# Kernel tuning notes

Measured on AMD Instinct MI355X. Metric: run time of the kernel, lower is better.

Reference implementation:

```python
import jax, jax.numpy as jnp
import numpy as np

VOCAB = 32000
WDIM = 768      # bert-base hidden size, per self.w_dim
H = 512         # lstm_hidden
NUM_CAT = 5
START = 3       # l2ind['SOS']
END = 4         # l2ind['EOS']
T = 2048
NEG = -10000.0


def _lstm_dir(x, Wih, Whh, bih, bhh, reverse):
    # x: [T, WDIM]; torch LSTM gate order: i, f, g, o
    z_in = x @ Wih.T + bih + bhh  # [T, 4H] precompute input projection
    def step(carry, zt):
        h, c = carry
        z = zt + h @ Whh.T
        i, f, g, o = jnp.split(z, 4)
        c = jax.nn.sigmoid(f) * c + jax.nn.sigmoid(i) * jnp.tanh(g)
        h = jax.nn.sigmoid(o) * jnp.tanh(c)
        return (h, c), h
    init = (jnp.zeros((H,), x.dtype), jnp.zeros((H,), x.dtype))
    _, hs = jax.lax.scan(step, init, z_in, reverse=reverse)
    return hs  # [T, H], aligned with input order


def setup_inputs():
    key = jax.random.key(0)
    ks = jax.random.split(key, 13)
    s = 0.05
    sent = jax.random.randint(ks[0], (T,), 0, VOCAB)
    emb = jax.random.normal(ks[1], (VOCAB, WDIM), jnp.float32) * 0.02
    Wih_f = jax.random.normal(ks[2], (4 * H, WDIM), jnp.float32) * s
    Whh_f = jax.random.normal(ks[3], (4 * H, H), jnp.float32) * s
    bih_f = jax.random.normal(ks[4], (4 * H,), jnp.float32) * s
    bhh_f = jax.random.normal(ks[5], (4 * H,), jnp.float32) * s
    Wih_b = jax.random.normal(ks[6], (4 * H, WDIM), jnp.float32) * s
    Whh_b = jax.random.normal(ks[7], (4 * H, H), jnp.float32) * s
    bih_b = jax.random.normal(ks[8], (4 * H,), jnp.float32) * s
    bhh_b = jax.random.normal(ks[9], (4 * H,), jnp.float32) * s
    fc_w = jax.random.normal(ks[10], (NUM_CAT, 2 * H), jnp.float32) * s
    fc_b = jax.random.normal(ks[11], (NUM_CAT,), jnp.float32) * s
    transitions = jax.random.normal(ks[12], (NUM_CAT, NUM_CAT), jnp.float32)
    transitions = transitions.at[START, :].set(NEG).at[:, END].set(NEG)
    return {"sent": sent, "emb": emb,
            "Wih_f": Wih_f, "Whh_f": Whh_f, "bih_f": bih_f, "bhh_f": bhh_f,
            "Wih_b": Wih_b, "Whh_b": Whh_b, "bih_b": bih_b, "bhh_b": bhh_b,
            "fc_w": fc_w, "fc_b": fc_b, "transitions": transitions}


def reference(sent, emb, Wih_f, Whh_f, bih_f, bhh_f, Wih_b, Whh_b, bih_b, bhh_b, fc_w, fc_b, transitions):
    # _get_scores: embedding -> BiLSTM -> fc
    x = emb[sent]                                   # [T, WDIM]
    h_f = _lstm_dir(x, Wih_f, Whh_f, bih_f, bhh_f, reverse=False)
    h_b = _lstm_dir(x, Wih_b, Whh_b, bih_b, bhh_b, reverse=True)
    out = jnp.concatenate([h_f, h_b], axis=-1)      # [T, 2H]
    feats = out @ fc_w.T + fc_b                     # [T, NUM_CAT]

    # _viterbi_decode: transitions[i, j] = score of moving from tag j to tag i
    init = feats[0] + transitions[:, START]         # [NUM_CAT]
    def vstep(layer, feat_t):
        # scores[i, j] = feat_t[i] + transitions[i, j] + layer[j]
        scores = feat_t[:, None] + transitions + layer[None, :]
        return jnp.max(scores, axis=1), jnp.argmax(scores, axis=1)
    layer, parents = jax.lax.scan(vstep, init, feats[1:])  # parents: [T-1, NUM_CAT]

    final = layer + transitions[END]
    idx0 = jnp.argmax(final)
    path_score = jnp.max(final)

    # backtrack (parents[0] of the original loop is all-START and gets popped)
    def btrack(idx, p):
        nxt = p[idx]
        return nxt, nxt
    _, idxs = jax.lax.scan(btrack, idx0, parents, reverse=True)  # [T-1]
    path = jnp.concatenate([idxs, idx0[None]])      # [T]
    return path, path_score
```

## Files before the change

### kernel.cpp

```cpp
#include <hip/hip_runtime.h>

#define TT 2048
#define WD 768
#define HH 512
#define G4 2048
#define NC 5
#define SENT 0xFFFFFFFFu

typedef float f4 __attribute__((ext_vector_type(4)));
typedef unsigned int u4 __attribute__((ext_vector_type(4)));

__global__ __launch_bounds__(256, 1) void fused_main(
    const int* __restrict__ sent, const float* __restrict__ emb,
    const float* __restrict__ Wih_f, const float* __restrict__ bih_f, const float* __restrict__ bhh_f,
    const float* __restrict__ Wih_b, const float* __restrict__ bih_b, const float* __restrict__ bhh_b,
    const float* __restrict__ Whh_f, const float* __restrict__ Whh_b,
    float* __restrict__ zin_f, float* __restrict__ zin_b,
    unsigned int* __restrict__ hw_f, unsigned int* __restrict__ hw_b,
    unsigned int* __restrict__ zcnt)
{
    __shared__ float As[16][128];
    __shared__ float Bs[16][128];
    __shared__ float hs[HH];
    __shared__ float zb[256];

    const int tid = threadIdx.x;

    if (blockIdx.x >= 64) {
        const int lin  = blockIdx.x - 64;
        const int pair = lin >> 5;
        const int sub  = lin & 31;
        const int dirn = sub & 1;
        const int gx   = sub >> 1;
        const int ty   = dirn ? (15 - pair) : pair;

        const float* Wih = dirn ? Wih_b : Wih_f;
        const float* bih = dirn ? bih_b : bih_f;
        const float* bhh = dirn ? bhh_b : bhh_f;
        float* zin = dirn ? zin_b : zin_f;

        const int t0 = ty * 128;
        const int g0 = gx * 128;
        const int tm = tid >> 4, tn = tid & 15;

        float acc[8][8];
#pragma unroll
        for (int a = 0; a < 8; a++)
#pragma unroll
            for (int b = 0; b < 8; b++) acc[a][b] = 0.f;

        for (int kt = 0; kt < 48; ++kt) {
            const int k0 = kt * 16;
#pragma unroll
            for (int u = 0; u < 2; ++u) {
                const int s = tid * 2 + u;
                const int m = s >> 2, kq = s & 3;
                const int rowA = sent[t0 + m];
                float4 av = *(const float4*)(emb + (size_t)rowA * WD + k0 + kq * 4);
                As[kq * 4 + 0][m] = av.x; As[kq * 4 + 1][m] = av.y;
                As[kq * 4 + 2][m] = av.z; As[kq * 4 + 3][m] = av.w;
                float4 bv = *(const float4*)(Wih + (size_t)(g0 + m) * WD + k0 + kq * 4);
                Bs[kq * 4 + 0][m] = bv.x; Bs[kq * 4 + 1][m] = bv.y;
                Bs[kq * 4 + 2][m] = bv.z; Bs[kq * 4 + 3][m] = bv.w;
            }
            __syncthreads();
#pragma unroll
            for (int kk = 0; kk < 16; ++kk) {
                float4 a0 = *(const float4*)&As[kk][tm * 8];
                float4 a1 = *(const float4*)&As[kk][tm * 8 + 4];
                float4 b0 = *(const float4*)&Bs[kk][tn * 8];
                float4 b1 = *(const float4*)&Bs[kk][tn * 8 + 4];
                float av8[8] = {a0.x, a0.y, a0.z, a0.w, a1.x, a1.y, a1.z, a1.w};
                float bv8[8] = {b0.x, b0.y, b0.z, b0.w, b1.x, b1.y, b1.z, b1.w};
#pragma unroll
                for (int a = 0; a < 8; a++)
#pragma unroll
                    for (int b = 0; b < 8; b++) acc[a][b] += av8[a] * bv8[b];
            }
            __syncthreads();
        }
        float bias[8];
#pragma unroll
        for (int b = 0; b < 8; b++) { int g = g0 + tn * 8 + b; bias[b] = bih[g] + bhh[g]; }
#pragma unroll
        for (int a = 0; a < 8; a++) {
            const int t = t0 + tm * 8 + a;
            float* op = zin + (size_t)t * G4 + g0 + tn * 8;
            f4 o0 = {acc[a][0] + bias[0], acc[a][1] + bias[1], acc[a][2] + bias[2], acc[a][3] + bias[3]};
            f4 o1 = {acc[a][4] + bias[4], acc[a][5] + bias[5], acc[a][6] + bias[6], acc[a][7] + bias[7]};
            asm volatile("global_store_dwordx4 %0, %1, off sc1" :: "v"(op), "v"(o0) : "memory");
            asm volatile("global_store_dwordx4 %0, %1, off sc1" :: "v"(op + 4), "v"(o1) : "memory");
        }
        __syncthreads();
        if (tid == 0) atomicAdd(&zcnt[dirn * 16 + ty], 1u);
        return;
    }

    const int bid = blockIdx.x;
    const int d = bid >> 5;
    const int k = bid & 31;
    const float* zin = d ? zin_b : zin_f;
    const float* Whh = d ? Whh_b : Whh_f;
    unsigned int* hw = d ? hw_b : hw_f;

    const int q = tid >> 6;
    const int r = tid & 63;
    const int gate = r >> 4, jj = r & 15;
    const int grow = gate * HH + k * 16 + jj;

    const f4* wp = (const f4*)(Whh + (size_t)grow * HH + q * 128);
    f4 w[32];
#pragma unroll
    for (int i = 0; i < 32; ++i) w[i] = wp[i];
#pragma unroll
    for (int i = 0; i < 32; ++i)
        asm volatile("" : "+a"(w[i]));

    float c = 0.f;
    const int l = tid;
    const int g = l >> 4, j = l & 15;
    const int n16 = k * 16 + j;

    int readyty = -1;

    for (int it = 0; it < TT; ++it) {
        const int t = d ? (TT - 1 - it) : it;

        float z = 0.f;
        if (tid < 64) {
            const int tyc = t >> 7;
            if (tyc != readyty) {
                const unsigned int* cp = zcnt + d * 16 + tyc;
                unsigned int cv;
                do {
                    asm volatile("global_load_dword %0, %1, off sc0 sc1\n\t"
                                 "s_waitcnt vmcnt(0)"
                                 : "=v"(cv) : "v"(cp) : "memory");
                } while (cv < 16u);
                readyty = tyc;
            }
            z = zin[(size_t)t * G4 + g * HH + n16];
        }

        if (it > 0 && tid < 64) {
            const int tp = d ? (t + 1) : (t - 1);
            const unsigned int* pa = hw + (size_t)tp * HH + l * 8;
            u4 a0, a1;
            for (;;) {
                asm volatile(
                    "global_load_dwordx4 %0, %2, off sc0 sc1\n\t"
                    "global_load_dwordx4 %1, %2, off offset:16 sc0 sc1\n\t"
                    "s_waitcnt vmcnt(0)"
                    : "=v"(a0), "=v"(a1) : "v"(pa) : "memory");
                if (a0.x != SENT && a0.y != SENT && a0.z != SENT && a0.w != SENT &&
                    a1.x != SENT && a1.y != SENT && a1.z != SENT && a1.w != SENT) break;
            }
            u4* hd = (u4*)(hs + l * 8);
            hd[0] = a0; hd[1] = a1;
        }
        __syncthreads();

#pragma unroll
        for (int i = 0; i < 32; ++i) asm volatile("" : "+a"(w[i]));

        float part = 0.f;
        if (it > 0) {
            const f4* hv = ((const f4*)hs) + (q << 5);
#pragma unroll
            for (int i = 0; i < 32; ++i) {
                f4 h4 = hv[i];
                part += w[i].x * h4.x + w[i].y * h4.y + w[i].z * h4.z + w[i].w * h4.w;
            }
        }
        zb[tid] = part;
        __syncthreads();

        if (tid < 64) {
            float s = zb[l] + zb[64 + l] + zb[128 + l] + zb[192 + l];
            const float pre = z + s;
            float act;
            if (g == 2) act = tanhf(pre);
            else        act = 1.f / (1.f + expf(-pre));
            const float gi = __shfl(act, j);
            const float gf = __shfl(act, j + 16);
            const float gg = __shfl(act, j + 32);
            const float go = __shfl(act, j + 48);
            if (l < 16) {
                c = gf * c + gi * gg;
                const float hval = go * tanhf(c);
                __hip_atomic_store(&hw[(size_t)t * HH + k * 16 + l],
                                   __float_as_uint(hval),
                                   __ATOMIC_RELAXED, __HIP_MEMORY_SCOPE_AGENT);
            }
        }
    }
}

__global__ void feats_kernel(const float* __restrict__ h_f, const float* __restrict__ h_b,
                             const float* __restrict__ fc_w, const float* __restrict__ fc_b,
                             float* __restrict__ feats)
{
    const int t = blockIdx.x;
    const int l = threadIdx.x;
    float acc[NC] = {0.f, 0.f, 0.f, 0.f, 0.f};
    for (int m = 0; m < 16; ++m) {
        const int cg = l + m * 64;
        const float hv = (cg < HH) ? h_f[(size_t)t * HH + cg]
                                   : h_b[(size_t)t * HH + cg - HH];
#pragma unroll
        for (int i = 0; i < NC; i++) acc[i] += hv * fc_w[i * (2 * HH) + cg];
    }
#pragma unroll
    for (int i = 0; i < NC; i++) {
#pragma unroll
        for (int off = 32; off; off >>= 1) acc[i] += __shfl_xor(acc[i], off);
    }
    if (l == 0) {
#pragma unroll
        for (int i = 0; i < NC; i++) feats[(size_t)t * NC + i] = acc[i] + fc_b[i];
    }
}

__global__ void viterbi_kernel(const float* __restrict__ feats,
                               const float* __restrict__ trans,
                               float* __restrict__ out)
{
    __shared__ float fs[TT * NC];
    __shared__ int par[TT];
    __shared__ float pathv[TT];
    const int tid = threadIdx.x;
    for (int i = tid; i < TT * NC; i += 64) fs[i] = feats[i];
    float tr[25];
#pragma unroll
    for (int i = 0; i < 25; i++) tr[i] = trans[i];
    __syncthreads();

    float layer[NC];
#pragma unroll
    for (int i = 0; i < NC; i++) layer[i] = fs[i] + tr[i * 5 + 3];

    for (int s = 0; s < TT - 1; ++s) {
        const float* ft = &fs[(s + 1) * NC];
        float nl[NC]; int pk = 0;
#pragma unroll
        for (int i = 0; i < NC; i++) {
            float best = tr[i * 5 + 0] + layer[0]; int bj = 0;
#pragma unroll
            for (int jj = 1; jj < NC; jj++) {
                const float v = tr[i * 5 + jj] + layer[jj];
                if (v > best) { best = v; bj = jj; }
            }
            nl[i] = ft[i] + best;
            pk |= bj << (3 * i);
        }
#pragma unroll
        for (int i = 0; i < NC; i++) layer[i] = nl[i];
        if (tid == 0) par[s] = pk;
    }
    float best = layer[0] + tr[20]; int idx0 = 0;
#pragma unroll
    for (int jj = 1; jj < NC; jj++) {
        const float v = layer[jj] + tr[20 + jj];
        if (v > best) { best = v; idx0 = jj; }
    }
    __syncthreads();
    if (tid == 0) {
        pathv[TT - 1] = (float)idx0;
        int idx = idx0;
        for (int s = TT - 2; s >= 0; --s) {
            idx = (par[s] >> (3 * idx)) & 7;
            pathv[s] = (float)idx;
        }
        out[TT] = best;
    }
    __syncthreads();
    for (int i = tid; i < TT; i += 64) out[i] = pathv[i];
}

extern "C" void kernel_launch(void* const* d_in, const int* in_sizes, int n_in,
                              void* d_out, int out_size, void* d_ws, size_t ws_size,
                              hipStream_t stream) {
    const int*   sent   = (const int*)d_in[0];
    const float* emb    = (const float*)d_in[1];
    const float* Wih_f  = (const float*)d_in[2];
    const float* Whh_f  = (const float*)d_in[3];
    const float* bih_f  = (const float*)d_in[4];
    const float* bhh_f  = (const float*)d_in[5];
    const float* Wih_b  = (const float*)d_in[6];
    const float* Whh_b  = (const float*)d_in[7];
    const float* bih_b  = (const float*)d_in[8];
    const float* bhh_b  = (const float*)d_in[9];
    const float* fc_w   = (const float*)d_in[10];
    const float* fc_b   = (const float*)d_in[11];
    const float* trans  = (const float*)d_in[12];
    float* out = (float*)d_out;

    char* ws = (char*)d_ws;
    float* zin_f = (float*)ws;
    float* zin_b = (float*)(ws + (size_t)16777216);
    unsigned int* hw_f = (unsigned int*)(ws + (size_t)33554432);
    unsigned int* hw_b = (unsigned int*)(ws + (size_t)37748736);
    float* feats = (float*)(ws + (size_t)41943040);
    unsigned int* zcnt = (unsigned int*)(ws + (size_t)42008576);

    hipMemsetAsync(hw_f, 0xFF, (size_t)8388608, stream);
    hipMemsetAsync(zcnt, 0, (size_t)128, stream);

    fused_main<<<576, 256, 0, stream>>>(sent, emb,
                                        Wih_f, bih_f, bhh_f,
                                        Wih_b, bih_b, bhh_b,
                                        Whh_f, Whh_b,
                                        zin_f, zin_b, hw_f, hw_b, zcnt);

    feats_kernel<<<TT, 64, 0, stream>>>((const float*)hw_f, (const float*)hw_b,
                                        fc_w, fc_b, feats);

    viterbi_kernel<<<1, 64, 0, stream>>>(feats, trans, out);
}
```

Measured before the change: 4.781 ms.

## Fuse fc projection into recurrent kernel and parallelize Viterbi backtrack

The recurrent workgroups, once their timesteps are done, spin-wait on the sentinel-filled h buffers and compute the fc feats for a slice of timesteps, which removes the separate feats kernel launch. The Viterbi forward loop prefetches the next step's features into registers. Backtracking becomes a two-level parallel scheme: each of 64 lanes composes parent maps over 32 steps, one lane chains the composed maps, then all lanes fill in their segments. The risks are the spin-polling tail in the main kernel and the extra register pressure from the per-lane parent arrays.

```diff
diff --git a/kernel.cpp b/kernel.cpp
--- a/kernel.cpp
+++ b/kernel.cpp
@@ -17,7 +17,9 @@
     const float* __restrict__ Whh_f, const float* __restrict__ Whh_b,
     float* __restrict__ zin_f, float* __restrict__ zin_b,
     unsigned int* __restrict__ hw_f, unsigned int* __restrict__ hw_b,
-    unsigned int* __restrict__ zcnt)
+    unsigned int* __restrict__ zcnt,
+    const float* __restrict__ fc_w, const float* __restrict__ fc_b,
+    float* __restrict__ feats)
 {
     __shared__ float As[16][128];
     __shared__ float Bs[16][128];
@@ -194,30 +196,60 @@
             }
         }
     }
-}
-
-__global__ void feats_kernel(const float* __restrict__ h_f, const float* __restrict__ h_b,
-                             const float* __restrict__ fc_w, const float* __restrict__ fc_b,
-                             float* __restrict__ feats)
-{
-    const int t = blockIdx.x;
-    const int l = threadIdx.x;
-    float acc[NC] = {0.f, 0.f, 0.f, 0.f, 0.f};
-    for (int m = 0; m < 16; ++m) {
-        const int cg = l + m * 64;
-        const float hv = (cg < HH) ? h_f[(size_t)t * HH + cg]
-                                   : h_b[(size_t)t * HH + cg - HH];
-#pragma unroll
-        for (int i = 0; i < NC; i++) acc[i] += hv * fc_w[i * (2 * HH) + cg];
-    }
-#pragma unroll
-    for (int i = 0; i < NC; i++) {
-#pragma unroll
-        for (int off = 32; off; off >>= 1) acc[i] += __shfl_xor(acc[i], off);
-    }
-    if (l == 0) {
-#pragma unroll
-        for (int i = 0; i < NC; i++) feats[(size_t)t * NC + i] = acc[i] + fc_b[i];
+
+    {
+        const int wgid = d * 32 + k;
+        float* const rowbuf = (q < 2) ? (&As[0][0] + q * 1024)
+                                      : (&Bs[0][0] + (q - 2) * 1024);
+        for (int n = 0; n < 8; ++n) {
+            const int t = (wgid * 4 + q) * 8 + n;
+            {
+                const unsigned int* pa = hw_f + (size_t)t * HH + r * 8;
+                u4 a0, a1;
+                for (;;) {
+                    asm volatile(
+                        "global_load_dwordx4 %0, %2, off sc0 sc1\n\t"
+                        "global_load_dwordx4 %1, %2, off offset:16 sc0 sc1\n\t"
+                        "s_waitcnt vmcnt(0)"
+                        : "=v"(a0), "=v"(a1) : "v"(pa) : "memory");
+                    if (a0.x != SENT && a0.y != SENT && a0.z != SENT && a0.w != SENT &&
+                        a1.x != SENT && a1.y != SENT && a1.z != SENT && a1.w != SENT) break;
+                }
+                u4* dstp = (u4*)(rowbuf + r * 8);
+                dstp[0] = a0; dstp[1] = a1;
+            }
+            {
+                const unsigned int* pa = hw_b + (size_t)t * HH + r * 8;
+                u4 a0, a1;
+                for (;;) {
+                    asm volatile(
+                        "global_load_dwordx4 %0, %2, off sc0 sc1\n\t"
+                        "global_load_dwordx4 %1, %2, off offset:16 sc0 sc1\n\t"
+                        "s_waitcnt vmcnt(0)"
+                        : "=v"(a0), "=v"(a1) : "v"(pa) : "memory");
+                    if (a0.x != SENT && a0.y != SENT && a0.z != SENT && a0.w != SENT &&
+                        a1.x != SENT && a1.y != SENT && a1.z != SENT && a1.w != SENT) break;
+                }
+                u4* dstp = (u4*)(rowbuf + HH + r * 8);
+                dstp[0] = a0; dstp[1] = a1;
+            }
+            float facc[NC] = {0.f, 0.f, 0.f, 0.f, 0.f};
+            for (int m = 0; m < 16; ++m) {
+                const int cg = r + m * 64;
+                const float hv = rowbuf[cg];
+#pragma unroll
+                for (int i = 0; i < NC; i++) facc[i] += hv * fc_w[i * (2 * HH) + cg];
+            }
+#pragma unroll
+            for (int i = 0; i < NC; i++) {
+#pragma unroll
+                for (int off = 32; off; off >>= 1) facc[i] += __shfl_xor(facc[i], off);
+            }
+            if (r == 0) {
+#pragma unroll
+                for (int i = 0; i < NC; i++) feats[(size_t)t * NC + i] = facc[i] + fc_b[i];
+            }
+        }
     }
 }
 
@@ -228,6 +260,8 @@
     __shared__ float fs[TT * NC];
     __shared__ int par[TT];
     __shared__ float pathv[TT];
+    __shared__ unsigned int maps[64];
+    __shared__ int bidx[64];
     const int tid = threadIdx.x;
     for (int i = tid; i < TT * NC; i += 64) fs[i] = feats[i];
     float tr[25];
@@ -239,8 +273,16 @@
 #pragma unroll
     for (int i = 0; i < NC; i++) layer[i] = fs[i] + tr[i * 5 + 3];
 
+    float ftc[NC];
+#pragma unroll
+    for (int i = 0; i < NC; i++) ftc[i] = fs[1 * NC + i];
+
     for (int s = 0; s < TT - 1; ++s) {
-        const float* ft = &fs[(s + 1) * NC];
+        const int sp = (s + 2 < TT) ? (s + 2) : (TT - 1);
+        float ftn[NC];
+#pragma unroll
+        for (int i = 0; i < NC; i++) ftn[i] = fs[sp * NC + i];
+
         float nl[NC]; int pk = 0;
 #pragma unroll
         for (int i = 0; i < NC; i++) {
@@ -250,11 +292,11 @@
                 const float v = tr[i * 5 + jj] + layer[jj];
                 if (v > best) { best = v; bj = jj; }
             }
-            nl[i] = ft[i] + best;
+            nl[i] = ftc[i] + best;
             pk |= bj << (3 * i);
         }
 #pragma unroll
-        for (int i = 0; i < NC; i++) layer[i] = nl[i];
+        for (int i = 0; i < NC; i++) { layer[i] = nl[i]; ftc[i] = ftn[i]; }
         if (tid == 0) par[s] = pk;
     }
     float best = layer[0] + tr[20]; int idx0 = 0;
@@ -264,15 +306,43 @@
         if (v > best) { best = v; idx0 = jj; }
     }
     __syncthreads();
+
+    const int slo = tid * 32;
+    const int shi0 = slo + 31;
+    const int shi = (shi0 < TT - 1) ? shi0 : (TT - 2);
+    int preg[32];
+#pragma unroll
+    for (int u = 0; u < 32; ++u) {
+        int su = slo + u; if (su > TT - 2) su = TT - 2;
+        preg[u] = par[su];
+    }
+    int m0 = 0, m1 = 1, m2 = 2, m3 = 3, m4 = 4;
+    for (int s = shi; s >= slo; --s) {
+        const int pv = preg[s - slo];
+        m0 = (pv >> (3 * m0)) & 7;
+        m1 = (pv >> (3 * m1)) & 7;
+        m2 = (pv >> (3 * m2)) & 7;
+        m3 = (pv >> (3 * m3)) & 7;
+        m4 = (pv >> (3 * m4)) & 7;
+    }
+    maps[tid] = (unsigned)(m0 | (m1 << 3) | (m2 << 6) | (m3 << 9) | (m4 << 12));
+    __syncthreads();
     if (tid == 0) {
-        pathv[TT - 1] = (float)idx0;
-        int idx = idx0;
-        for (int s = TT - 2; s >= 0; --s) {
-            idx = (par[s] >> (3 * idx)) & 7;
-            pathv[s] = (float)idx;
-        }
-        out[TT] = best;
-    }
+        int e = idx0;
+        for (int cc = 63; cc >= 0; --cc) {
+            bidx[cc] = e;
+            e = (int)((maps[cc] >> (3 * e)) & 7u);
+        }
+    }
+    __syncthreads();
+    {
+        int e = bidx[tid];
+        for (int s = shi; s >= slo; --s) {
+            e = (preg[s - slo] >> (3 * e)) & 7;
+            pathv[s] = (float)e;
+        }
+    }
+    if (tid == 0) { pathv[TT - 1] = (float)idx0; out[TT] = best; }
     __syncthreads();
     for (int i = tid; i < TT; i += 64) out[i] = pathv[i];
 }
@@ -310,9 +380,7 @@
                                         Wih_f, bih_f, bhh_f,
                                         Wih_b, bih_b, bhh_b,
                                         Whh_f, Whh_b,
-                                        zin_f, zin_b, hw_f, hw_b, zcnt);
-
-    feats_kernel<<<TT, 64, 0, stream>>>((const float*)hw_f, (const float*)hw_b,
+                                        zin_f, zin_b, hw_f, hw_b, zcnt,
                                         fc_w, fc_b, feats);
 
     viterbi_kernel<<<1, 64, 0, stream>>>(feats, trans, out);
```

New measurement: 4.729 ms. About the same (-1.1%).
